# Kernel tuning notes

Hardware: AMD Instinct MI355X
Metric: run time of the kernel (lower is better)

Reference implementation:

```python
import jax, jax.numpy as jnp
import numpy as np

N_EXPERTS = 48
D_IN = 2 * 1280 * 8 * 8  # 163840
D_OUT = 2


def setup_inputs() -> dict:
    key = jax.random.key(0)
    k_x, k_t, k_w, k_b = jax.random.split(key, 4)
    B = 512
    x = jax.random.normal(k_x, (B, 2, 1280, 8, 8), dtype=jnp.float32)
    t = jax.random.randint(k_t, (B,), 0, N_EXPERTS)  # torch code uses t[i]-1; neg index wraps
    # nn.Linear default init: U(-1/sqrt(fan_in), 1/sqrt(fan_in))
    bound = 1.0 / np.sqrt(D_IN)
    W = jax.random.uniform(k_w, (N_EXPERTS, D_IN, D_OUT), dtype=jnp.float32,
                           minval=-bound, maxval=bound)
    b = jax.random.uniform(k_b, (N_EXPERTS, D_OUT), dtype=jnp.float32,
                           minval=-bound, maxval=bound)
    return {"x": x, "t": t, "W": W, "b": b}


def reference(x, t, W, b):
    # x: [B, 2, 1280, 8, 8] -> [B, D_IN]; per-sample expert indexed by t-1
    B = x.shape[0]
    xf = x.reshape(B, -1)  # [B, D_IN]
    idx = (t - 1) % N_EXPERTS  # matches torch negative indexing for t=0
    Wg = W[idx]  # [B, D_IN, D_OUT]
    bg = b[idx]  # [B, D_OUT]
    out = jnp.einsum('bd,bdk->bk', xf, Wg) + bg  # [B, D_OUT]
    return out
```

## Files before the change

kernel.cpp:

```cpp
#include <hip/hip_runtime.h>

#define N_EXPERTS 48
#define D_IN 163840
#define D_OUT 2
#define BATCH 512
#define SPLIT 8
#define CHUNK (D_IN / SPLIT)
#define THREADS 256
#define ITERS (CHUNK / 4 / THREADS)

__global__ void init_out_kernel(const int* __restrict__ t,
                                const float* __restrict__ b,
                                float* __restrict__ out) {
    int i = blockIdx.x * blockDim.x + threadIdx.x;
    if (i < BATCH * D_OUT) {
        int s = i >> 1;
        int k = i & 1;
        int e = (t[s] + N_EXPERTS - 1) % N_EXPERTS;
        out[i] = b[e * D_OUT + k];
    }
}

__global__ __launch_bounds__(THREADS) void moe_dot_kernel(
        const float* __restrict__ x,
        const int* __restrict__ t,
        const float* __restrict__ W,
        float* __restrict__ out) {
    const int chunk  = blockIdx.x;
    const int sample = blockIdx.y;

    const int e = (t[sample] + N_EXPERTS - 1) % N_EXPERTS;

    const float4* __restrict__ xp =
        (const float4*)(x + (size_t)sample * D_IN + (size_t)chunk * CHUNK);
    const float4* __restrict__ wp =
        (const float4*)(W + (size_t)e * D_IN * D_OUT + (size_t)chunk * CHUNK * D_OUT);

    float acc0 = 0.f, acc1 = 0.f;

#pragma unroll
    for (int it = 0; it < ITERS; ++it) {
        const int i = it * THREADS + threadIdx.x;
        float4 xv = xp[i];
        float4 w0 = wp[2 * i];
        float4 w1 = wp[2 * i + 1];
        acc0 += xv.x * w0.x + xv.y * w0.z + xv.z * w1.x + xv.w * w1.z;
        acc1 += xv.x * w0.y + xv.y * w0.w + xv.z * w1.y + xv.w * w1.w;
    }

    for (int off = 32; off > 0; off >>= 1) {
        acc0 += __shfl_down(acc0, off);
        acc1 += __shfl_down(acc1, off);
    }

    __shared__ float s0[THREADS / 64];
    __shared__ float s1[THREADS / 64];
    const int wid  = threadIdx.x >> 6;
    const int lane = threadIdx.x & 63;
    if (lane == 0) { s0[wid] = acc0; s1[wid] = acc1; }
    __syncthreads();

    if (threadIdx.x == 0) {
        float a0 = s0[0] + s0[1] + s0[2] + s0[3];
        float a1 = s1[0] + s1[1] + s1[2] + s1[3];
        atomicAdd(&out[sample * D_OUT + 0], a0);
        atomicAdd(&out[sample * D_OUT + 1], a1);
    }
}

extern "C" void kernel_launch(void* const* d_in, const int* in_sizes, int n_in,
                              void* d_out, int out_size, void* d_ws, size_t ws_size,
                              hipStream_t stream) {
    const float* x = (const float*)d_in[0];
    const int*   t = (const int*)d_in[1];
    const float* W = (const float*)d_in[2];
    const float* b = (const float*)d_in[3];
    float* out = (float*)d_out;

    init_out_kernel<<<(BATCH * D_OUT + THREADS - 1) / THREADS, THREADS, 0, stream>>>(
        t, b, out);

    dim3 grid(SPLIT, BATCH);
    moe_dot_kernel<<<grid, THREADS, 0, stream>>>(x, t, W, out);
}
```

Before: 492.7 us.

## Sort samples by expert and stream x with nontemporal loads

Adds a bucketing kernel that groups samples by their expert index, so consecutive blocks process samples sharing the same expert weights and W reuse in L2/MALL improves. The activation x, which is read only once, is loaded with nontemporal hints so it does not evict weight lines. The unroll factor also drops from full to 4. This adds an extra single-block kernel launch, and the sorted order relies on blocks being dispatched roughly in blockIdx order.

```diff
diff --git a/kernel.cpp b/kernel.cpp
--- a/kernel.cpp
+++ b/kernel.cpp
@@ -8,6 +8,28 @@
 #define CHUNK (D_IN / SPLIT)
 #define THREADS 256
 #define ITERS (CHUNK / 4 / THREADS)
+
+typedef float nfloat4 __attribute__((ext_vector_type(4)));
+
+__global__ __launch_bounds__(BATCH) void bucket_kernel(const int* __restrict__ t,
+                                                       int* __restrict__ ws) {
+    __shared__ int cnt[N_EXPERTS];
+    __shared__ int off[N_EXPERTS];
+    const int s = threadIdx.x;
+    if (s < N_EXPERTS) cnt[s] = 0;
+    __syncthreads();
+    const int e = (t[s] + N_EXPERTS - 1) % N_EXPERTS;
+    const int rank = atomicAdd(&cnt[e], 1);
+    __syncthreads();
+    if (s == 0) {
+        int acc = 0;
+        for (int i = 0; i < N_EXPERTS; ++i) { off[i] = acc; acc += cnt[i]; }
+    }
+    __syncthreads();
+    const int slot = off[e] + rank;
+    ws[slot] = s;
+    ws[BATCH + slot] = e;
+}
 
 __global__ void init_out_kernel(const int* __restrict__ t,
                                 const float* __restrict__ b,
@@ -23,25 +45,25 @@
 
 __global__ __launch_bounds__(THREADS) void moe_dot_kernel(
         const float* __restrict__ x,
-        const int* __restrict__ t,
+        const int* __restrict__ ws,
         const float* __restrict__ W,
         float* __restrict__ out) {
-    const int chunk  = blockIdx.x;
-    const int sample = blockIdx.y;
+    const int chunk = blockIdx.x;
+    const int slot  = blockIdx.y;
+    const int sample = ws[slot];
+    const int e      = ws[BATCH + slot];
 
-    const int e = (t[sample] + N_EXPERTS - 1) % N_EXPERTS;
-
-    const float4* __restrict__ xp =
-        (const float4*)(x + (size_t)sample * D_IN + (size_t)chunk * CHUNK);
+    const nfloat4* __restrict__ xp =
+        (const nfloat4*)(x + (size_t)sample * D_IN + (size_t)chunk * CHUNK);
     const float4* __restrict__ wp =
         (const float4*)(W + (size_t)e * D_IN * D_OUT + (size_t)chunk * CHUNK * D_OUT);
 
     float acc0 = 0.f, acc1 = 0.f;
 
-#pragma unroll
+#pragma unroll 4
     for (int it = 0; it < ITERS; ++it) {
         const int i = it * THREADS + threadIdx.x;
-        float4 xv = xp[i];
+        nfloat4 xv = __builtin_nontemporal_load(&xp[i]);
         float4 w0 = wp[2 * i];
         float4 w1 = wp[2 * i + 1];
         acc0 += xv.x * w0.x + xv.y * w0.z + xv.z * w1.x + xv.w * w1.z;
@@ -76,10 +98,13 @@
     const float* W = (const float*)d_in[2];
     const float* b = (const float*)d_in[3];
     float* out = (float*)d_out;
+    int* ws = (int*)d_ws;
+
+    bucket_kernel<<<1, BATCH, 0, stream>>>(t, ws);
 
     init_out_kernel<<<(BATCH * D_OUT + THREADS - 1) / THREADS, THREADS, 0, stream>>>(
         t, b, out);
 
     dim3 grid(SPLIT, BATCH);
-    moe_dot_kernel<<<grid, THREADS, 0, stream>>>(x, t, W, out);
+    moe_dot_kernel<<<grid, THREADS, 0, stream>>>(x, ws, W, out);
 }
```

Result: faster. 480.8 us (-2.4%).
